# Performance work log

Hardware: AMD Instinct MI355X
Metric: run time of the kernel (lower is better)

The kernel has to match this reference:

```python
import jax, jax.numpy as jnp
import numpy as np

N, C, H, W = 512, 256, 14, 14
EPS = 1e-5


def _conv(x, w, pad):
    # x: [N,C,H,W], w: [O,I,kh,kw]
    return jax.lax.conv_general_dilated(
        x, w, window_strides=(1, 1), padding=[(pad, pad), (pad, pad)],
        dimension_numbers=("NCHW", "OIHW", "NCHW"))


def setup_inputs() -> dict:
    key = jax.random.key(0)
    ks = jax.random.split(key, 12)
    x = jax.random.normal(ks[0], (N, C, H, W), jnp.float32)
    gc = jax.random.normal(ks[1], (N, C, H, W), jnp.float32)
    # valid boxes: xmin,ymin in [0,800), w,h in [20,170)
    xy = jax.random.uniform(ks[2], (N, 2), jnp.float32) * 800.0
    wh = jax.random.uniform(ks[3], (N, 2), jnp.float32) * 150.0 + 20.0
    boxes = jnp.concatenate([xy, xy + wh], axis=1)
    classes = jax.random.randint(ks[4], (N,), 0, 2, jnp.int32)
    s3 = 1.0 / np.sqrt(C * 9)
    s1 = 1.0 / np.sqrt(C)
    Wc3 = jax.random.normal(ks[5], (C, C, 3, 3), jnp.float32) * s3
    Wc1 = jax.random.normal(ks[6], (C, C, 1, 1), jnp.float32) * s1
    Wt3 = jax.random.normal(ks[7], (C, C, 3, 3), jnp.float32) * s3
    Wt1 = jax.random.normal(ks[8], (C, C, 1, 1), jnp.float32) * s1
    Wf3 = jax.random.normal(ks[9], (C, C, 3, 3), jnp.float32) * s3
    Wf1 = jax.random.normal(ks[10], (C, C, 1, 1), jnp.float32) * s1
    bn_gamma = jnp.ones((C,), jnp.float32)
    bn_beta = jnp.zeros((C,), jnp.float32)
    bn_mean = jnp.zeros((C,), jnp.float32)
    bn_var = jnp.ones((C,), jnp.float32)
    return dict(x=x, global_context=gc, boxes=boxes, classes=classes,
                Wc3=Wc3, Wc1=Wc1, Wt3=Wt3, Wt1=Wt1, Wf3=Wf3, Wf1=Wf1,
                bn_gamma=bn_gamma, bn_beta=bn_beta, bn_mean=bn_mean, bn_var=bn_var)


def reference(x, global_context, boxes, classes, Wc3, Wc1, Wt3, Wt1, Wf3, Wf1,
              bn_gamma, bn_beta, bn_mean, bn_var):
    # pairwise intersection / self-area gating
    area = (boxes[:, 2] - boxes[:, 0]) * (boxes[:, 3] - boxes[:, 1])  # [N]
    lt = jnp.maximum(boxes[:, None, :2], boxes[None, :, :2])  # [N,N,2]
    rb = jnp.minimum(boxes[:, None, 2:], boxes[None, :, 2:])
    wh = jnp.clip(rb - lt, 0.0)
    inter = wh[..., 0] * wh[..., 1]                            # [N,N]
    inter_percent = inter / area[None, :]                      # divide by area of box j
    mask = (inter_percent > 0.9).astype(x.dtype)               # [N,N]; diag always 1
    counts = mask.sum(axis=1)                                  # [N] >= 1
    # per-instance gather-average of member features
    avg = jnp.einsum("ij,jchw->ichw", mask, x) / counts[:, None, None, None]
    text_in = jnp.where((counts > 1.0)[:, None, None, None], avg, x)
    # branch convs (batched instead of per-proposal loop)
    char_out = _conv(_conv(x, Wc3, 1), Wc1, 0)
    text_out = _conv(_conv(text_in, Wt3, 1), Wt1, 0)
    char_context = jnp.where((classes != 0)[:, None, None, None], char_out, text_out)
    fuse = char_context + x + global_context
    y = _conv(_conv(fuse, Wf3, 1), Wf1, 0)
    inv = jax.lax.rsqrt(bn_var + EPS)
    y = (y - bn_mean[None, :, None, None]) * (bn_gamma * inv)[None, :, None, None] \
        + bn_beta[None, :, None, None]
    return jax.nn.relu(y)
```

## Files before the change

### kernel.cpp

```cpp
#include <hip/hip_runtime.h>

typedef unsigned short u16;
typedef unsigned int u32;
typedef __bf16 bf16x8 __attribute__((ext_vector_type(8)));
typedef float f32x4 __attribute__((ext_vector_type(4)));
typedef u16 u16x4 __attribute__((ext_vector_type(4)));
typedef u16 u16x8 __attribute__((ext_vector_type(8)));
typedef float f4v __attribute__((ext_vector_type(4)));

#define NB   512
#define CCH  256
#define HW   196
#define LROW 40
#define ACT_ELEMS (197 * LROW)
#define WLDS_ELEMS (9 * 64 * 32)
#define SSTR 53248
#define CGSTR 147456

__device__ inline u16 f2bf(float f) {
    u32 u = __float_as_uint(f);
    u32 r = (u + 0x7FFFu + ((u >> 16) & 1u)) >> 16;
    return (u16)r;
}

__global__ void wconv_kernel(const float* __restrict__ Wc3, const float* __restrict__ Wt3,
                             const float* __restrict__ Wf3, const float* __restrict__ Wc1,
                             const float* __restrict__ Wt1, const float* __restrict__ Wf1,
                             u16* __restrict__ w3, u16* __restrict__ w1o)
{
    int bid = blockIdx.x, tid = threadIdx.x;
    if (bid < 768) {
        int wset = bid >> 8;
        int co = bid & 255;
        int cgi = co >> 6, cop = co & 63;
        int cc = tid >> 5, cip = tid & 31;
        const float* src = wset == 0 ? Wc3 : (wset == 1 ? Wt3 : Wf3);
#pragma unroll
        for (int rs = 0; rs < 9; ++rs) {
            float v = src[(co * 256 + tid) * 9 + rs];
            w3[wset * 589824 + cgi * CGSTR + (cc * 9 + rs) * 2048 + cop * 32 + cip] = f2bf(v);
        }
    } else {
        int k = (bid - 768) * 256 + tid;
        int wsel = k >> 14;
        int rem = k & 16383;
        const float* src = wsel == 0 ? Wc1 : (wsel == 1 ? Wt1 : Wf1);
        f4v v = *(const f4v*)(src + rem * 4);
        u16x4 o = { f2bf(v.x), f2bf(v.y), f2bf(v.z), f2bf(v.w) };
        *(u16x4*)(w1o + wsel * 65536 + rem * 4) = o;
    }
}

__global__ void mask_kernel(const float* __restrict__ boxes, int* __restrict__ counts,
                            int* __restrict__ members)
{
    int i = blockIdx.x;
    int ln = threadIdx.x;
    __shared__ int cnt;
    if (ln == 0) cnt = 0;
    __syncthreads();
    float xi0 = boxes[i * 4 + 0], yi0 = boxes[i * 4 + 1];
    float xi1 = boxes[i * 4 + 2], yi1 = boxes[i * 4 + 3];
    for (int j = ln; j < NB; j += 64) {
        float xj0 = boxes[j * 4 + 0], yj0 = boxes[j * 4 + 1];
        float xj1 = boxes[j * 4 + 2], yj1 = boxes[j * 4 + 3];
        float areaj = (xj1 - xj0) * (yj1 - yj0);
        float lx = fmaxf(xi0, xj0), ly = fmaxf(yi0, yj0);
        float rx = fminf(xi1, xj1), ry = fminf(yi1, yj1);
        float w = fmaxf(rx - lx, 0.f), h = fmaxf(ry - ly, 0.f);
        if (w * h / areaj > 0.9f) {
            int p = atomicAdd(&cnt, 1);
            members[i * NB + p] = j;
        }
    }
    __syncthreads();
    if (ln == 0) counts[i] = cnt;
}

__global__ void bin_kernel(const float* __restrict__ x, const int* __restrict__ classes,
                           const int* __restrict__ counts, const int* __restrict__ members,
                           u16* __restrict__ bin)
{
    const int s = blockIdx.x, tid = threadIdx.x;
    const int cnt = counts[s];
    u16* binS = bin + s * SSTR;
    if (classes[s] != 0 || cnt <= 1) {
        for (int v = tid; v < 64 * 208; v += 256) {
            int c4 = v / 208;
            int px = v - c4 * 208;
            u16x4 o = {0, 0, 0, 0};
            if (px < HW) {
#pragma unroll
                for (int rg = 0; rg < 4; ++rg)
                    o[rg] = f2bf(x[(s * CCH + c4 * 4 + rg) * HW + px]);
            }
            *(u16x4*)(binS + (c4 * 208 + px) * 4) = o;
        }
    } else {
        __shared__ int mem[NB];
        for (int u = tid; u < cnt; u += 256) mem[u] = members[s * NB + u];
        __syncthreads();
        const float inv = 1.f / (float)cnt;
        for (int v = tid; v < 64 * 208; v += 256) {
            int c4 = v / 208;
            int px = v - c4 * 208;
            u16x4 o = {0, 0, 0, 0};
            if (px < HW) {
                float a[4] = {0.f, 0.f, 0.f, 0.f};
                for (int k = 0; k < cnt; ++k) {
                    const float* xm = x + mem[k] * (CCH * HW);
#pragma unroll
                    for (int rg = 0; rg < 4; ++rg)
                        a[rg] += xm[(c4 * 4 + rg) * HW + px];
                }
#pragma unroll
                for (int rg = 0; rg < 4; ++rg) o[rg] = f2bf(a[rg] * inv);
            }
            *(u16x4*)(binS + (c4 * 208 + px) * 4) = o;
        }
    }
}

__global__ __launch_bounds__(256, 3) void conv3x3_kernel(
    const u16* __restrict__ in, u16* __restrict__ out,
    const u16* __restrict__ w0, const u16* __restrict__ w1,
    const int* __restrict__ classes, int useClass)
{
    __shared__ u16 lds[ACT_ELEMS + WLDS_ELEMS];
    const int tid = threadIdx.x;
    const int bid = blockIdx.x;
    const int s  = bid >> 2;
    const int cg = bid & 3;
    const int wv = tid >> 6;
    const int ln = tid & 63;
    const int q = ln >> 4;
    const int l15 = ln & 15;
    const int t0 = (wv == 0) ? 0 : (wv == 1 ? 4 : (wv == 2 ? 7 : 10));
    const int NT = (wv == 0) ? 4 : 3;

    const u16* wsel = (((useClass && classes[s] == 0) ? w1 : w0)) + cg * CGSTR;

    if (tid < 20) ((u32*)lds)[196 * (LROW / 2) + tid] = 0u;

    int baddr[4], vbits[4];
#pragma unroll
    for (int t = 0; t < 4; ++t) {
        int px = (t0 + t) * 16 + l15;
        int vb = 0;
        int ba = 196 * LROW + q * 8;
        if (t < NT && px < HW) {
            int y = px / 14;
            int x = px - y * 14;
            ba = px * LROW + q * 8;
#pragma unroll
            for (int rs = 0; rs < 9; ++rs) {
                int iy = y + rs / 3 - 1;
                int ix = x + rs % 3 - 1;
                if (iy >= 0 && iy < 14 && ix >= 0 && ix < 14) vb |= 1 << rs;
            }
        }
        baddr[t] = ba;
        vbits[t] = vb;
    }

    f32x4 acc[4][4];
#pragma unroll
    for (int a = 0; a < 4; ++a)
#pragma unroll
        for (int t = 0; t < 4; ++t) acc[a][t] = (f32x4){0.f, 0.f, 0.f, 0.f};

    const u16* inS = in + s * SSTR;

    for (int cc = 0; cc < 8; ++cc) {
        __syncthreads();
        for (int v = tid; v < 1568; v += 256) {
            int ci4 = v & 7;
            int px = v >> 3;
            u16x4 val = *(const u16x4*)(inS + ((cc * 8 + ci4) * 208 + px) * 4);
            *(u16x4*)(lds + px * LROW + ci4 * 4) = val;
        }
        {
            const u16* wcc = wsel + cc * WLDS_ELEMS;
#pragma unroll
            for (int k = 0; k < 9; ++k) {
                int idx = tid + k * 256;
                *(u16x8*)(lds + ACT_ELEMS + idx * 8) = *(const u16x8*)(wcc + idx * 8);
            }
        }
        __syncthreads();

#pragma unroll
        for (int rs = 0; rs < 9; ++rs) {
            const int d = (rs / 3 - 1) * 14 + (rs % 3 - 1);
            bf16x8 af[4];
#pragma unroll
            for (int sub = 0; sub < 4; ++sub)
                af[sub] = *(const bf16x8*)(lds + ACT_ELEMS + rs * 2048 + (sub * 16 + l15) * 32 + q * 8);
#pragma unroll
            for (int t = 0; t < 4; ++t) {
                if (t < NT) {
                    int addr = ((vbits[t] >> rs) & 1) ? (baddr[t] + d * LROW)
                                                      : (196 * LROW + q * 8);
                    bf16x8 b = *(const bf16x8*)(lds + addr);
#pragma unroll
                    for (int sub = 0; sub < 4; ++sub)
                        acc[sub][t] = __builtin_amdgcn_mfma_f32_16x16x32_bf16(af[sub], b, acc[sub][t], 0, 0, 0);
                }
            }
        }
    }

#pragma unroll
    for (int sub = 0; sub < 4; ++sub) {
        int co4 = cg * 16 + sub * 4 + q;
#pragma unroll
        for (int t = 0; t < 4; ++t) {
            if (t < NT) {
                int pxs = (t0 + t) * 16 + l15;
                u16x4 o = { f2bf(acc[sub][t][0]), f2bf(acc[sub][t][1]),
                            f2bf(acc[sub][t][2]), f2bf(acc[sub][t][3]) };
                *(u16x4*)(out + (s * (size_t)SSTR) + (co4 * 208 + pxs) * 4) = o;
            }
        }
    }
}

template <int MODE>
__global__ __launch_bounds__(256, 3) void conv1x1_kernel(
    const u16* __restrict__ in, const u16* __restrict__ w0, const u16* __restrict__ w1,
    const int* __restrict__ classes, int useClass,
    const float* __restrict__ xin, const float* __restrict__ gcin,
    const float* __restrict__ gamma, const float* __restrict__ beta,
    const float* __restrict__ mean, const float* __restrict__ var,
    void* __restrict__ outv)
{
    __shared__ u16 lds[ACT_ELEMS];
    const int tid = threadIdx.x;
    const int bid = blockIdx.x;
    const int s  = bid >> 2;
    const int cg = bid & 3;
    const int wv = tid >> 6;
    const int ln = tid & 63;
    const int q = ln >> 4;
    const int l15 = ln & 15;
    const int t0 = (wv == 0) ? 0 : (wv == 1 ? 4 : (wv == 2 ? 7 : 10));
    const int NT = (wv == 0) ? 4 : 3;

    const u16* wsel = (useClass && classes[s] == 0) ? w1 : w0;

    if (tid < 20) ((u32*)lds)[196 * (LROW / 2) + tid] = 0u;

    int baddr[4];
#pragma unroll
    for (int t = 0; t < 4; ++t) {
        int px = (t0 + t) * 16 + l15;
        baddr[t] = (t < NT && px < HW ? px : 196) * LROW + q * 8;
    }

    f32x4 acc[4][4];
#pragma unroll
    for (int a = 0; a < 4; ++a)
#pragma unroll
        for (int t = 0; t < 4; ++t) acc[a][t] = (f32x4){0.f, 0.f, 0.f, 0.f};

    const u16* inS = in + s * SSTR;

    for (int cc = 0; cc < 8; ++cc) {
        __syncthreads();
        for (int v = tid; v < 1568; v += 256) {
            int ci4 = v & 7;
            int px = v >> 3;
            u16x4 val = *(const u16x4*)(inS + ((cc * 8 + ci4) * 208 + px) * 4);
            *(u16x4*)(lds + px * LROW + ci4 * 4) = val;
        }
        __syncthreads();

        bf16x8 af[4];
#pragma unroll
        for (int sub = 0; sub < 4; ++sub)
            af[sub] = *(const bf16x8*)(wsel + ((cg * 64 + sub * 16 + l15) * 256 + cc * 32 + q * 8));
#pragma unroll
        for (int t = 0; t < 4; ++t) {
            if (t < NT) {
                bf16x8 b = *(const bf16x8*)(lds + baddr[t]);
#pragma unroll
                for (int sub = 0; sub < 4; ++sub)
                    acc[sub][t] = __builtin_amdgcn_mfma_f32_16x16x32_bf16(af[sub], b, acc[sub][t], 0, 0, 0);
            }
        }
    }

    if (MODE == 0) {
        u16* outb = (u16*)outv;
#pragma unroll
        for (int sub = 0; sub < 4; ++sub) {
            int co4 = cg * 16 + sub * 4 + q;
#pragma unroll
            for (int t = 0; t < 4; ++t) {
                if (t < NT) {
                    int pxs = (t0 + t) * 16 + l15;
                    u16x4 o = {0, 0, 0, 0};
                    if (pxs < HW) {
#pragma unroll
                        for (int rg = 0; rg < 4; ++rg) {
                            int idx = (s * CCH + co4 * 4 + rg) * HW + pxs;
                            o[rg] = f2bf(acc[sub][t][rg] + xin[idx] + gcin[idx]);
                        }
                    }
                    *(u16x4*)(outb + (s * (size_t)SSTR) + (co4 * 208 + pxs) * 4) = o;
                }
            }
        }
    } else {
        float* outf = (float*)outv;
        float scl[4][4], mn[4][4], bt[4][4];
#pragma unroll
        for (int sub = 0; sub < 4; ++sub)
#pragma unroll
            for (int rg = 0; rg < 4; ++rg) {
                int c = cg * 64 + sub * 16 + q * 4 + rg;
                scl[sub][rg] = gamma[c] * rsqrtf(var[c] + 1e-5f);
                mn[sub][rg] = mean[c];
                bt[sub][rg] = beta[c];
            }
#pragma unroll
        for (int sub = 0; sub < 4; ++sub)
#pragma unroll
            for (int t = 0; t < 4; ++t) {
                if (t < NT) {
                    int pxs = (t0 + t) * 16 + l15;
                    if (pxs < HW) {
#pragma unroll
                        for (int rg = 0; rg < 4; ++rg) {
                            int co = cg * 64 + sub * 16 + q * 4 + rg;
                            float v = (acc[sub][t][rg] - mn[sub][rg]) * scl[sub][rg] + bt[sub][rg];
                            outf[(s * CCH + co) * HW + pxs] = fmaxf(v, 0.f);
                        }
                    }
                }
            }
    }
}

extern "C" void kernel_launch(void* const* d_in, const int* in_sizes, int n_in,
                              void* d_out, int out_size, void* d_ws, size_t ws_size,
                              hipStream_t stream)
{
    const float* x    = (const float*)d_in[0];
    const float* gc   = (const float*)d_in[1];
    const float* boxes= (const float*)d_in[2];
    const int*   cls  = (const int*)d_in[3];
    const float* Wc3  = (const float*)d_in[4];
    const float* Wc1  = (const float*)d_in[5];
    const float* Wt3  = (const float*)d_in[6];
    const float* Wt1  = (const float*)d_in[7];
    const float* Wf3  = (const float*)d_in[8];
    const float* Wf1  = (const float*)d_in[9];
    const float* gam  = (const float*)d_in[10];
    const float* bet  = (const float*)d_in[11];
    const float* mea  = (const float*)d_in[12];
    const float* var  = (const float*)d_in[13];
    float* out = (float*)d_out;
    char* ws = (char*)d_ws;

    u16* w3      = (u16*)(ws);
    u16* w1o     = (u16*)(ws + 3538944);
    int* counts  = (int*)(ws + 3932160);
    int* members = (int*)(ws + 3934208);
    u16* bufA    = (u16*)(ws + 4982784);
    u16* bufB    = (u16*)(ws + 59508736);

    wconv_kernel<<<960, 256, 0, stream>>>(Wc3, Wt3, Wf3, Wc1, Wt1, Wf1, w3, w1o);
    mask_kernel<<<512, 64, 0, stream>>>(boxes, counts, members);
    bin_kernel<<<512, 256, 0, stream>>>(x, cls, counts, members, bufA);
    conv3x3_kernel<<<2048, 256, 0, stream>>>(bufA, bufB, w3, w3 + 589824, cls, 1);
    conv1x1_kernel<0><<<2048, 256, 0, stream>>>(bufB, w1o, w1o + 65536, cls, 1, x, gc,
                                                nullptr, nullptr, nullptr, nullptr, (void*)bufA);
    conv3x3_kernel<<<2048, 256, 0, stream>>>(bufA, bufB, w3 + 2 * 589824, w3, cls, 0);
    conv1x1_kernel<1><<<2048, 256, 0, stream>>>(bufB, w1o + 2 * 65536, w1o, cls, 0, nullptr, nullptr,
                                                gam, bet, mea, var, (void*)out);
}
```

Baseline: 872.4 us.

## Read conv3x3 weights directly from global memory and widen bin_kernel vectorization

The conv3x3 kernel no longer stages weight tiles in LDS each channel chunk. It loads the A fragments straight from global (L2-cached) memory using a new [rs][co][ci] weight layout produced by wconv_kernel. This removes the LDS weight copy and shrinks shared memory per block, which may allow more resident blocks, at the cost of global-latency loads inside the MFMA loop. Separately, bin_kernel is split across 4x more blocks and uses float4 loads with 8-wide bf16 stores.

After: 1.228 ms. +40.8%, slower.

```diff
diff --git a/kernel.cpp b/kernel.cpp
--- a/kernel.cpp
+++ b/kernel.cpp
@@ -13,9 +13,7 @@
 #define HW   196
 #define LROW 40
 #define ACT_ELEMS (197 * LROW)
-#define WLDS_ELEMS (9 * 64 * 32)
 #define SSTR 53248
-#define CGSTR 147456
 
 __device__ inline u16 f2bf(float f) {
     u32 u = __float_as_uint(f);
@@ -32,13 +30,11 @@
     if (bid < 768) {
         int wset = bid >> 8;
         int co = bid & 255;
-        int cgi = co >> 6, cop = co & 63;
-        int cc = tid >> 5, cip = tid & 31;
         const float* src = wset == 0 ? Wc3 : (wset == 1 ? Wt3 : Wf3);
 #pragma unroll
         for (int rs = 0; rs < 9; ++rs) {
             float v = src[(co * 256 + tid) * 9 + rs];
-            w3[wset * 589824 + cgi * CGSTR + (cc * 9 + rs) * 2048 + cop * 32 + cip] = f2bf(v);
+            w3[wset * 589824 + (rs * 256 + co) * 256 + tid] = f2bf(v);
         }
     } else {
         int k = (bid - 768) * 256 + tid;
@@ -77,47 +73,60 @@
     if (ln == 0) counts[i] = cnt;
 }
 
-__global__ void bin_kernel(const float* __restrict__ x, const int* __restrict__ classes,
-                           const int* __restrict__ counts, const int* __restrict__ members,
-                           u16* __restrict__ bin)
-{
-    const int s = blockIdx.x, tid = threadIdx.x;
+__global__ __launch_bounds__(256) void bin_kernel(
+    const float* __restrict__ x, const int* __restrict__ classes,
+    const int* __restrict__ counts, const int* __restrict__ members,
+    u16* __restrict__ bin)
+{
+    const int s = blockIdx.x >> 2;
+    const int ch = blockIdx.x & 3;
+    const int tid = threadIdx.x;
     const int cnt = counts[s];
     u16* binS = bin + s * SSTR;
-    if (classes[s] != 0 || cnt <= 1) {
-        for (int v = tid; v < 64 * 208; v += 256) {
-            int c4 = v / 208;
-            int px = v - c4 * 208;
-            u16x4 o = {0, 0, 0, 0};
-            if (px < HW) {
-#pragma unroll
-                for (int rg = 0; rg < 4; ++rg)
-                    o[rg] = f2bf(x[(s * CCH + c4 * 4 + rg) * HW + px]);
-            }
-            *(u16x4*)(binS + (c4 * 208 + px) * 4) = o;
-        }
-    } else {
-        __shared__ int mem[NB];
+    const bool avg = (classes[s] == 0 && cnt > 1);
+    __shared__ int mem[NB];
+    if (avg) {
         for (int u = tid; u < cnt; u += 256) mem[u] = members[s * NB + u];
         __syncthreads();
-        const float inv = 1.f / (float)cnt;
-        for (int v = tid; v < 64 * 208; v += 256) {
-            int c4 = v / 208;
-            int px = v - c4 * 208;
-            u16x4 o = {0, 0, 0, 0};
-            if (px < HW) {
-                float a[4] = {0.f, 0.f, 0.f, 0.f};
+    }
+    const float inv = avg ? (1.f / (float)cnt) : 1.f;
+    for (int v = tid; v < 832; v += 256) {
+        int c4 = ch * 16 + v / 52;
+        int p4 = (v - (v / 52) * 52) * 4;
+        u16x8 o0 = {0,0,0,0,0,0,0,0}, o1 = {0,0,0,0,0,0,0,0};
+        if (p4 < HW) {
+            float a[4][4];
+#pragma unroll
+            for (int rg = 0; rg < 4; ++rg)
+#pragma unroll
+                for (int j = 0; j < 4; ++j) a[rg][j] = 0.f;
+            if (!avg) {
+#pragma unroll
+                for (int rg = 0; rg < 4; ++rg) {
+                    f4v r = *(const f4v*)(x + (s * CCH + c4 * 4 + rg) * HW + p4);
+                    a[rg][0] = r.x; a[rg][1] = r.y; a[rg][2] = r.z; a[rg][3] = r.w;
+                }
+            } else {
                 for (int k = 0; k < cnt; ++k) {
                     const float* xm = x + mem[k] * (CCH * HW);
 #pragma unroll
-                    for (int rg = 0; rg < 4; ++rg)
-                        a[rg] += xm[(c4 * 4 + rg) * HW + px];
-                }
-#pragma unroll
-                for (int rg = 0; rg < 4; ++rg) o[rg] = f2bf(a[rg] * inv);
-            }
-            *(u16x4*)(binS + (c4 * 208 + px) * 4) = o;
-        }
+                    for (int rg = 0; rg < 4; ++rg) {
+                        f4v r = *(const f4v*)(xm + (c4 * 4 + rg) * HW + p4);
+                        a[rg][0] += r.x; a[rg][1] += r.y; a[rg][2] += r.z; a[rg][3] += r.w;
+                    }
+                }
+#pragma unroll
+                for (int rg = 0; rg < 4; ++rg)
+#pragma unroll
+                    for (int j = 0; j < 4; ++j) a[rg][j] *= inv;
+            }
+            o0[0] = f2bf(a[0][0]); o0[1] = f2bf(a[1][0]); o0[2] = f2bf(a[2][0]); o0[3] = f2bf(a[3][0]);
+            o0[4] = f2bf(a[0][1]); o0[5] = f2bf(a[1][1]); o0[6] = f2bf(a[2][1]); o0[7] = f2bf(a[3][1]);
+            o1[0] = f2bf(a[0][2]); o1[1] = f2bf(a[1][2]); o1[2] = f2bf(a[2][2]); o1[3] = f2bf(a[3][2]);
+            o1[4] = f2bf(a[0][3]); o1[5] = f2bf(a[1][3]); o1[6] = f2bf(a[2][3]); o1[7] = f2bf(a[3][3]);
+        }
+        *(u16x8*)(binS + (c4 * 208 + p4) * 4) = o0;
+        *(u16x8*)(binS + (c4 * 208 + p4) * 4 + 8) = o1;
     }
 }
 
@@ -126,7 +135,7 @@
     const u16* __restrict__ w0, const u16* __restrict__ w1,
     const int* __restrict__ classes, int useClass)
 {
-    __shared__ u16 lds[ACT_ELEMS + WLDS_ELEMS];
+    __shared__ u16 lds[ACT_ELEMS];
     const int tid = threadIdx.x;
     const int bid = blockIdx.x;
     const int s  = bid >> 2;
@@ -138,7 +147,7 @@
     const int t0 = (wv == 0) ? 0 : (wv == 1 ? 4 : (wv == 2 ? 7 : 10));
     const int NT = (wv == 0) ? 4 : 3;
 
-    const u16* wsel = (((useClass && classes[s] == 0) ? w1 : w0)) + cg * CGSTR;
+    const u16* wsel = (useClass && classes[s] == 0) ? w1 : w0;
 
     if (tid < 20) ((u32*)lds)[196 * (LROW / 2) + tid] = 0u;
 
@@ -179,14 +188,6 @@
             u16x4 val = *(const u16x4*)(inS + ((cc * 8 + ci4) * 208 + px) * 4);
             *(u16x4*)(lds + px * LROW + ci4 * 4) = val;
         }
-        {
-            const u16* wcc = wsel + cc * WLDS_ELEMS;
-#pragma unroll
-            for (int k = 0; k < 9; ++k) {
-                int idx = tid + k * 256;
-                *(u16x8*)(lds + ACT_ELEMS + idx * 8) = *(const u16x8*)(wcc + idx * 8);
-            }
-        }
         __syncthreads();
 
 #pragma unroll
@@ -195,7 +196,7 @@
             bf16x8 af[4];
 #pragma unroll
             for (int sub = 0; sub < 4; ++sub)
-                af[sub] = *(const bf16x8*)(lds + ACT_ELEMS + rs * 2048 + (sub * 16 + l15) * 32 + q * 8);
+                af[sub] = *(const bf16x8*)(wsel + ((rs * 256 + cg * 64 + sub * 16 + l15) * 256 + cc * 32 + q * 8));
 #pragma unroll
             for (int t = 0; t < 4; ++t) {
                 if (t < NT) {
@@ -372,7 +373,7 @@
 
     wconv_kernel<<<960, 256, 0, stream>>>(Wc3, Wt3, Wf3, Wc1, Wt1, Wf1, w3, w1o);
     mask_kernel<<<512, 64, 0, stream>>>(boxes, counts, members);
-    bin_kernel<<<512, 256, 0, stream>>>(x, cls, counts, members, bufA);
+    bin_kernel<<<2048, 256, 0, stream>>>(x, cls, counts, members, bufA);
     conv3x3_kernel<<<2048, 256, 0, stream>>>(bufA, bufB, w3, w3 + 589824, cls, 1);
     conv1x1_kernel<0><<<2048, 256, 0, stream>>>(bufB, w1o, w1o + 65536, cls, 1, x, gc,
                                                 nullptr, nullptr, nullptr, nullptr, (void*)bufA);
```
